# Kernel tuning notes

Measured on AMD Instinct MI355X. Metric: run time of the kernel, lower is better.

The kernel has to match this reference:

```python
import jax, jax.numpy as jnp
import numpy as np

NUM_QUBITS = 12
NUM_LAYERS = 4
N_CLASSES = 10
BATCH = 512
BN_EPS = 1e-5


def _apply_1q(state, U, wire):
    """Apply a 1-qubit gate U on `wire`. state: (B,)+(2,)*n; U: (2,2) or (B,2,2)."""
    state = jnp.moveaxis(state, wire + 1, -1)
    if U.ndim == 3:
        out = jnp.einsum('bij,b...j->b...i', U, state)
    else:
        out = jnp.einsum('ij,b...j->b...i', U, state)
    return jnp.moveaxis(out, -1, wire + 1)


def _apply_cnot(state, ctrl, tgt):
    s = jnp.moveaxis(state, (ctrl + 1, tgt + 1), (-2, -1))
    # where control bit == 1, flip the target axis
    s = jnp.concatenate([s[..., 0:1, :], s[..., 1:2, ::-1]], axis=-2)
    return jnp.moveaxis(s, (-2, -1), (ctrl + 1, tgt + 1))


def _rot(phi, theta, omega):
    """PennyLane Rot(phi, theta, omega) = RZ(omega) RY(theta) RZ(phi)."""
    c = jnp.cos(theta / 2)
    s = jnp.sin(theta / 2)
    row0 = jnp.stack([jnp.exp(-1j * (phi + omega) / 2) * c,
                      -jnp.exp(1j * (phi - omega) / 2) * s])
    row1 = jnp.stack([jnp.exp(-1j * (phi - omega) / 2) * s,
                      jnp.exp(1j * (phi + omega) / 2) * c])
    return jnp.stack([row0, row1]).astype(jnp.complex64)


def _circuit(x, weights):
    """Batched state-vector sim of the data-reuploading VQC.
    x: (B, n_qubits) angles; weights: (L, n_qubits, 3). Returns (B, N_CLASSES) <Z_i>."""
    B = x.shape[0]
    state = jnp.zeros((B,) + (2,) * NUM_QUBITS, jnp.complex64)
    state = state.at[(slice(None),) + (0,) * NUM_QUBITS].set(1.0)
    half = (x * 0.5).astype(jnp.float32)
    for l in range(NUM_LAYERS):
        w = weights[l]
        # angle embedding (RY(x_q) on each wire) -- batched gate, differs per sample
        for q in range(NUM_QUBITS):
            c = jnp.cos(half[:, q])
            s = jnp.sin(half[:, q])
            U = jnp.stack([jnp.stack([c, -s], -1),
                           jnp.stack([s, c], -1)], -2).astype(jnp.complex64)  # (B,2,2)
            state = _apply_1q(state, U, q)
        # one StronglyEntangling layer: Rot per wire (shared across batch)
        for q in range(NUM_QUBITS):
            state = _apply_1q(state, _rot(w[q, 0], w[q, 1], w[q, 2]), q)
        # ring of CNOTs (range 1)
        for q in range(NUM_QUBITS):
            state = _apply_cnot(state, q, (q + 1) % NUM_QUBITS)
    probs = jnp.abs(state) ** 2  # (B,)+(2,)*n, float32
    all_axes = tuple(range(1, NUM_QUBITS + 1))
    expz = []
    for i in range(N_CLASSES):
        axes = tuple(a for a in all_axes if a != i + 1)
        p = probs.sum(axis=axes)  # (B, 2) marginal of qubit i
        expz.append(p[:, 0] - p[:, 1])
    return jnp.stack(expz, axis=-1)  # (B, N_CLASSES)


def setup_inputs() -> dict:
    key = jax.random.key(0)
    k1, k2 = jax.random.split(key)
    x = jax.random.normal(k1, (BATCH, NUM_QUBITS), dtype=jnp.float32)
    weights = 0.01 * jax.random.uniform(k2, (NUM_LAYERS, NUM_QUBITS, 3), dtype=jnp.float32)
    bias = jnp.zeros((N_CLASSES,), jnp.float32)
    gamma = jnp.ones((N_CLASSES,), jnp.float32)
    beta = jnp.zeros((N_CLASSES,), jnp.float32)
    return {"x": x, "weights": weights, "bias": bias, "gamma": gamma, "beta": beta}


def reference(x, weights, bias, gamma, beta):
    expz = _circuit(x, weights)
    probs = jax.nn.softmax(expz + bias, axis=-1)
    # BatchNorm1d (training mode): biased batch statistics, affine
    mu = probs.mean(axis=0)
    var = probs.var(axis=0)
    return (probs - mu) / jnp.sqrt(var + BN_EPS) * gamma + beta
```

## Files before the change

### kernel.cpp

```cpp
#include <hip/hip_runtime.h>
#include <math.h>

#define NQ 12
#define NL 4
#define NC 10
#define NB 512
#define BN_EPS 1e-5f

typedef float v2f __attribute__((ext_vector_type(2)));

__device__ __forceinline__ void bfly(v2f& A, v2f& B,
    v2f c0, v2f c1, v2f c2, v2f c3, v2f c4, v2f c5, v2f c6, v2f c7)
{
    const v2f As = A.yx, Bs = B.yx;
    const v2f An = __builtin_elementwise_fma(c0, A,
                   __builtin_elementwise_fma(c1, As,
                   __builtin_elementwise_fma(c2, B, c3 * Bs)));
    const v2f Bn = __builtin_elementwise_fma(c4, A,
                   __builtin_elementwise_fma(c5, As,
                   __builtin_elementwise_fma(c6, B, c7 * Bs)));
    A = An; B = Bn;
}

__global__ __launch_bounds__(256) void vqc_kernel(
    const float* __restrict__ x, const float* __restrict__ w,
    const float* __restrict__ bias, float* __restrict__ probs)
{
    __shared__ v2f buf[2][4096];
    __shared__ __align__(16) float gm[48][16];
    __shared__ float red[4*NC];

    const int b = blockIdx.x;
    const int t = threadIdx.x;

    if (t < 48) {
        const int l = t / NQ, q = t % NQ;
        const float xq = 0.5f * x[b*NQ + q];
        const float cx = cosf(xq), sx = sinf(xq);
        const int wi = (l*NQ + q)*3;
        const float phi = w[wi], tht = w[wi+1], om = w[wi+2];
        const float ct = cosf(0.5f*tht), st = sinf(0.5f*tht);
        const float aa = 0.5f*(phi + om), dd = 0.5f*(phi - om);
        const float ca = cosf(aa), sa = sinf(aa);
        const float cd = cosf(dd), sd = sinf(dd);
        const float u00r =  ca*ct, u00i = -sa*ct;
        const float u01r = -cd*st, u01i = -sd*st;
        const float u10r =  cd*st, u10i = -sd*st;
        const float u11r =  ca*ct, u11i =  sa*ct;
        const float m00r = u00r*cx + u01r*sx, m00i = u00i*cx + u01i*sx;
        const float m01r = u01r*cx - u00r*sx, m01i = u01i*cx - u00i*sx;
        const float m10r = u10r*cx + u11r*sx, m10i = u10i*cx + u11i*sx;
        const float m11r = u11r*cx - u10r*sx, m11i = u11i*cx - u10i*sx;
        float* gp = gm[t];
        gp[0]  =  m00r; gp[1]  = m00r;
        gp[2]  = -m00i; gp[3]  = m00i;
        gp[4]  =  m01r; gp[5]  = m01r;
        gp[6]  = -m01i; gp[7]  = m01i;
        gp[8]  =  m10r; gp[9]  = m10r;
        gp[10] = -m10i; gp[11] = m10i;
        gp[12] =  m11r; gp[13] = m11r;
        gp[14] = -m11i; gp[15] = m11i;
    }
    __syncthreads();

    v2f a[16];
    #pragma unroll
    for (int r = 0; r < 16; ++r) a[r] = (v2f){0.f, 0.f};
    if (t == 0) a[0].x = 1.f;

    const int tl = t & 15, th4 = t >> 4;
    const int phit = t ^ th4;
    const int vAB = (th4 << 8) | (tl ^ (th4 * 17));
    const int wBC = (tl << 8) | ((th4 ^ tl) * 17);

    const unsigned b0_ = t & 1u, b1_ = (t>>1)&1u, b2_ = (t>>2)&1u, b3_ = (t>>3)&1u,
                   b4_ = (t>>4)&1u, b5_ = (t>>5)&1u, b6_ = (t>>6)&1u, b7_ = (t>>7)&1u;
    const unsigned P7 = b7_, P6 = P7^b6_, P5 = P6^b5_, P4 = P5^b4_,
                   P3 = P4^b3_, P2 = P3^b2_, P1 = P2^b1_, T = P1^b0_;
    const unsigned base_j = ((T ^ b7_) << 11) | (P6 << 10) | (P5 << 9) | (P4 << 8)
                          | (P3 << 7) | (P2 << 6) | (P1 << 5) | (T << 4)
                          | (T ? 0xFu : 0u);
    const unsigned rA = (base_j >> 8) & 15u;
    const unsigned tA = base_j & 255u;
    const unsigned baseCA = (rA << 8) | ((tA ^ (tA >> 4)) ^ (rA * 17u));

    #define STAGE(base) \
        _Pragma("unroll") \
        for (int g = 0; g < 4; ++g) { \
            const v2f* cp = (const v2f*)gm[(base) + 3 - g]; \
            const v2f c0=cp[0],c1=cp[1],c2=cp[2],c3=cp[3], \
                      c4=cp[4],c5=cp[5],c6=cp[6],c7=cp[7]; \
            const int bit = 1 << g; \
            _Pragma("unroll") \
            for (int r0 = 0; r0 < 16; ++r0) \
                if (!(r0 & bit)) bfly(a[r0], a[r0|bit], c0,c1,c2,c3,c4,c5,c6,c7); \
        }

    int pb = 0;
    #pragma unroll
    for (int l = 0; l < NL; ++l) {
        STAGE(l*12)
        {
            v2f* bp = buf[pb]; pb ^= 1;
            #pragma unroll
            for (int r = 0; r < 16; ++r) bp[vAB ^ (r*17)] = a[r];
            __syncthreads();
            #pragma unroll
            for (int r = 0; r < 16; ++r) a[r] = bp[(r<<8) | (phit ^ (r*17))];
        }

        STAGE(l*12 + 4)
        {
            v2f* bp = buf[pb]; pb ^= 1;
            #pragma unroll
            for (int r = 0; r < 16; ++r) bp[wBC ^ r] = a[r];
            __syncthreads();
            #pragma unroll
            for (int r = 0; r < 16; ++r) a[r] = bp[(r<<8) | (phit ^ (r*17))];
        }

        STAGE(l*12 + 8)
        if (l < NL-1) {
            v2f* bp = buf[pb]; pb ^= 1;
            #pragma unroll
            for (int r = 0; r < 16; ++r) {
                const unsigned k3 = (r>>3)&1u;
                const unsigned k2 = k3 ^ ((r>>2)&1u);
                const unsigned k1 = k2 ^ ((r>>1)&1u);
                const unsigned k0 = k1 ^ (r&1u);
                const unsigned K  = (k3<<3)|(k2<<2)|(k1<<1)|k0;
                const unsigned d  = K ^ (k0 * 0x888u);
                bp[baseCA ^ d] = a[r];
            }
            __syncthreads();
            #pragma unroll
            for (int r = 0; r < 16; ++r) a[r] = bp[(r<<8) | (phit ^ (r*17))];
        }
    }

    const float S0 = (T ^ b7_) ? -1.f : 1.f;
    const float S1 = P6 ? -1.f : 1.f;
    const float S2 = P5 ? -1.f : 1.f;
    const float S3 = P4 ? -1.f : 1.f;
    const float S4 = P3 ? -1.f : 1.f;
    const float S5 = P2 ? -1.f : 1.f;
    const float S6 = P1 ? -1.f : 1.f;
    const float S7 = T  ? -1.f : 1.f;
    const float S8 = T  ? -1.f : 1.f;
    const float S9 = T  ? -1.f : 1.f;

    float acc[NC];
    #pragma unroll
    for (int c = 0; c < NC; ++c) acc[c] = 0.f;
    #pragma unroll
    for (int r = 0; r < 16; ++r) {
        const float p = a[r].x*a[r].x + a[r].y*a[r].y;
        const int r3 = (r>>3)&1, r2 = (r>>2)&1, r1 = (r>>1)&1, r0b = r&1;
        const int par = r3 ^ r2 ^ r1 ^ r0b;
        acc[0] += (par        ? -S0 : S0) * p;
        acc[1] += S1 * p;
        acc[2] += S2 * p;
        acc[3] += S3 * p;
        acc[4] += S4 * p;
        acc[5] += S5 * p;
        acc[6] += S6 * p;
        acc[7] += S7 * p;
        acc[8] += (r3         ? -S8 : S8) * p;
        acc[9] += ((r3 ^ r2)  ? -S9 : S9) * p;
    }
    #pragma unroll
    for (int off = 32; off >= 1; off >>= 1) {
        #pragma unroll
        for (int c = 0; c < NC; ++c)
            acc[c] += __shfl_down(acc[c], off, 64);
    }
    const int wave = t >> 6, lane = t & 63;
    if (lane == 0) {
        #pragma unroll
        for (int c = 0; c < NC; ++c) red[wave*NC + c] = acc[c];
    }
    __syncthreads();
    if (t == 0) {
        float ez[NC];
        float mx = -1e30f;
        #pragma unroll
        for (int c = 0; c < NC; ++c) {
            ez[c] = red[c] + red[NC + c] + red[2*NC + c] + red[3*NC + c] + bias[c];
            mx = fmaxf(mx, ez[c]);
        }
        float sum = 0.f;
        #pragma unroll
        for (int c = 0; c < NC; ++c) { ez[c] = expf(ez[c] - mx); sum += ez[c]; }
        const float inv = 1.f / sum;
        #pragma unroll
        for (int c = 0; c < NC; ++c) probs[b*NC + c] = ez[c] * inv;
    }
}

__global__ __launch_bounds__(256) void bn_kernel(
    float* __restrict__ probs, const float* __restrict__ gamma,
    const float* __restrict__ beta)
{
    const int c = blockIdx.x;
    const int t = threadIdx.x;
    const float v0 = probs[t*NC + c];
    const float v1 = probs[(t + 256)*NC + c];
    float s  = v0 + v1;
    float ss = v0*v0 + v1*v1;
    #pragma unroll
    for (int off = 32; off >= 1; off >>= 1) {
        s  += __shfl_down(s,  off, 64);
        ss += __shfl_down(ss, off, 64);
    }
    __shared__ float sm[8];
    __shared__ float stat[2];
    const int wave = t >> 6, lane = t & 63;
    if (lane == 0) { sm[wave] = s; sm[4 + wave] = ss; }
    __syncthreads();
    if (t == 0) {
        const float S  = sm[0] + sm[1] + sm[2] + sm[3];
        const float SS = sm[4] + sm[5] + sm[6] + sm[7];
        const float mu  = S * (1.f/512.f);
        const float var = SS * (1.f/512.f) - mu*mu;
        stat[0] = mu;
        stat[1] = 1.f / sqrtf(var + BN_EPS);
    }
    __syncthreads();
    const float mu = stat[0], inv = stat[1];
    const float g = gamma[c], bt = beta[c];
    probs[t*NC + c]         = (v0 - mu) * inv * g + bt;
    probs[(t + 256)*NC + c] = (v1 - mu) * inv * g + bt;
}

extern "C" void kernel_launch(void* const* d_in, const int* in_sizes, int n_in,
                              void* d_out, int out_size, void* d_ws, size_t ws_size,
                              hipStream_t stream) {
    const float* x     = (const float*)d_in[0];
    const float* w     = (const float*)d_in[1];
    const float* bias  = (const float*)d_in[2];
    const float* gamma = (const float*)d_in[3];
    const float* beta  = (const float*)d_in[4];
    float* out = (float*)d_out;

    vqc_kernel<<<NB, 256, 0, stream>>>(x, w, bias, out);
    bn_kernel<<<NC, 256, 0, stream>>>(out, gamma, beta);
}
```

Baseline: 86.91 us.

## Split state vector over 512 threads with 8 amplitudes each and radix-8 stages

Moves from 256 threads holding 16 amplitudes (radix-16 stages, three LDS transposes per layer) to 512 threads holding 8 amplitudes (radix-8 stages, four transposes per layer) with a new XOR swizzle. The CNOT-ring permutation is now computed with a prefix-XOR formula, and the final Z-expectation reduction is rebuilt around per-thread parity sums. The goal is more parallelism and lower register pressure per block, at the cost of one extra shared-memory round trip and barrier per layer.

```diff
diff --git a/kernel.cpp b/kernel.cpp
--- a/kernel.cpp
+++ b/kernel.cpp
@@ -22,13 +22,13 @@
     A = An; B = Bn;
 }
 
-__global__ __launch_bounds__(256) void vqc_kernel(
+__global__ __launch_bounds__(512, 4) void vqc_kernel(
     const float* __restrict__ x, const float* __restrict__ w,
     const float* __restrict__ bias, float* __restrict__ probs)
 {
     __shared__ v2f buf[2][4096];
     __shared__ __align__(16) float gm[48][16];
-    __shared__ float red[4*NC];
+    __shared__ float red[8*NC];
 
     const int b = blockIdx.x;
     const int t = threadIdx.x;
@@ -63,111 +63,100 @@
     }
     __syncthreads();
 
-    v2f a[16];
-    #pragma unroll
-    for (int r = 0; r < 16; ++r) a[r] = (v2f){0.f, 0.f};
+    v2f a[8];
+    #pragma unroll
+    for (int r = 0; r < 8; ++r) a[r] = (v2f){0.f, 0.f};
     if (t == 0) a[0].x = 1.f;
 
-    const int tl = t & 15, th4 = t >> 4;
-    const int phit = t ^ th4;
-    const int vAB = (th4 << 8) | (tl ^ (th4 * 17));
-    const int wBC = (tl << 8) | ((th4 ^ tl) * 17);
-
-    const unsigned b0_ = t & 1u, b1_ = (t>>1)&1u, b2_ = (t>>2)&1u, b3_ = (t>>3)&1u,
-                   b4_ = (t>>4)&1u, b5_ = (t>>5)&1u, b6_ = (t>>6)&1u, b7_ = (t>>7)&1u;
-    const unsigned P7 = b7_, P6 = P7^b6_, P5 = P6^b5_, P4 = P5^b4_,
-                   P3 = P4^b3_, P2 = P3^b2_, P1 = P2^b1_, T = P1^b0_;
-    const unsigned base_j = ((T ^ b7_) << 11) | (P6 << 10) | (P5 << 9) | (P4 << 8)
-                          | (P3 << 7) | (P2 << 6) | (P1 << 5) | (T << 4)
-                          | (T ? 0xFu : 0u);
-    const unsigned rA = (base_j >> 8) & 15u;
-    const unsigned tA = base_j & 255u;
-    const unsigned baseCA = (rA << 8) | ((tA ^ (tA >> 4)) ^ (rA * 17u));
-
-    #define STAGE(base) \
+    const unsigned tu = (unsigned)t;
+    const unsigned tw = tu >> 6;
+    const unsigned baseB = (tw << 9) | (tu & 63u);
+    const unsigned baseC = (tw << 9) | (((tu >> 3) & 7u) << 6) | (tu & 7u);
+    const unsigned baseD = (tw << 9) | (((tu >> 3) & 7u) << 6) | ((tu & 7u) << 3);
+
+#define SWZ(i) ((i) ^ (((i) >> 4) & 15u))
+
+    #define STAGE(gbase) \
         _Pragma("unroll") \
-        for (int g = 0; g < 4; ++g) { \
-            const v2f* cp = (const v2f*)gm[(base) + 3 - g]; \
+        for (int g = 0; g < 3; ++g) { \
+            const v2f* cp = (const v2f*)gm[(gbase) + 2 - g]; \
             const v2f c0=cp[0],c1=cp[1],c2=cp[2],c3=cp[3], \
                       c4=cp[4],c5=cp[5],c6=cp[6],c7=cp[7]; \
             const int bit = 1 << g; \
             _Pragma("unroll") \
-            for (int r0 = 0; r0 < 16; ++r0) \
+            for (int r0 = 0; r0 < 8; ++r0) \
                 if (!(r0 & bit)) bfly(a[r0], a[r0|bit], c0,c1,c2,c3,c4,c5,c6,c7); \
         }
 
+    #define TRANS(IOLD, INEW) { \
+        v2f* bp = buf[pb]; pb ^= 1; \
+        _Pragma("unroll") \
+        for (int r = 0; r < 8; ++r) { const unsigned i_ = (IOLD); bp[SWZ(i_)] = a[r]; } \
+        __syncthreads(); \
+        _Pragma("unroll") \
+        for (int r = 0; r < 8; ++r) { const unsigned i_ = (INEW); a[r] = bp[SWZ(i_)]; } \
+    }
+
     int pb = 0;
     #pragma unroll
     for (int l = 0; l < NL; ++l) {
         STAGE(l*12)
-        {
-            v2f* bp = buf[pb]; pb ^= 1;
-            #pragma unroll
-            for (int r = 0; r < 16; ++r) bp[vAB ^ (r*17)] = a[r];
-            __syncthreads();
-            #pragma unroll
-            for (int r = 0; r < 16; ++r) a[r] = bp[(r<<8) | (phit ^ (r*17))];
-        }
-
-        STAGE(l*12 + 4)
-        {
-            v2f* bp = buf[pb]; pb ^= 1;
-            #pragma unroll
-            for (int r = 0; r < 16; ++r) bp[wBC ^ r] = a[r];
-            __syncthreads();
-            #pragma unroll
-            for (int r = 0; r < 16; ++r) a[r] = bp[(r<<8) | (phit ^ (r*17))];
-        }
-
-        STAGE(l*12 + 8)
+        TRANS(((unsigned)r << 9) | tu, baseB | ((unsigned)r << 6))
+        STAGE(l*12 + 3)
+        TRANS(baseB | ((unsigned)r << 6), baseC | ((unsigned)r << 3))
+        STAGE(l*12 + 6)
+        TRANS(baseC | ((unsigned)r << 3), baseD | (unsigned)r)
+        STAGE(l*12 + 9)
         if (l < NL-1) {
             v2f* bp = buf[pb]; pb ^= 1;
             #pragma unroll
-            for (int r = 0; r < 16; ++r) {
-                const unsigned k3 = (r>>3)&1u;
-                const unsigned k2 = k3 ^ ((r>>2)&1u);
-                const unsigned k1 = k2 ^ ((r>>1)&1u);
-                const unsigned k0 = k1 ^ (r&1u);
-                const unsigned K  = (k3<<3)|(k2<<2)|(k1<<1)|k0;
-                const unsigned d  = K ^ (k0 * 0x888u);
-                bp[baseCA ^ d] = a[r];
+            for (int r = 0; r < 8; ++r) {
+                unsigned i_ = baseD | (unsigned)r;
+                unsigned S = i_ ^ (i_ >> 1);
+                S ^= S >> 2; S ^= S >> 4; S ^= S >> 8;
+                const unsigned j = S ^ ((S & 1u) << 11);
+                bp[SWZ(j)] = a[r];
             }
             __syncthreads();
             #pragma unroll
-            for (int r = 0; r < 16; ++r) a[r] = bp[(r<<8) | (phit ^ (r*17))];
+            for (int r = 0; r < 8; ++r) {
+                const unsigned i_ = ((unsigned)r << 9) | tu;
+                a[r] = bp[SWZ(i_)];
+            }
         }
     }
 
-    const float S0 = (T ^ b7_) ? -1.f : 1.f;
-    const float S1 = P6 ? -1.f : 1.f;
-    const float S2 = P5 ? -1.f : 1.f;
-    const float S3 = P4 ? -1.f : 1.f;
-    const float S4 = P3 ? -1.f : 1.f;
-    const float S5 = P2 ? -1.f : 1.f;
-    const float S6 = P1 ? -1.f : 1.f;
-    const float S7 = T  ? -1.f : 1.f;
-    const float S8 = T  ? -1.f : 1.f;
-    const float S9 = T  ? -1.f : 1.f;
-
+    const unsigned t8 = (tu >> 8) & 1u;
+    const unsigned Q7 = t8 ^ ((tu >> 7) & 1u);
+    const unsigned Q6 = Q7 ^ ((tu >> 6) & 1u);
+    const unsigned Q5 = Q6 ^ ((tu >> 5) & 1u);
+    const unsigned Q4 = Q5 ^ ((tu >> 4) & 1u);
+    const unsigned Q3 = Q4 ^ ((tu >> 3) & 1u);
+    const unsigned Q2 = Q3 ^ ((tu >> 2) & 1u);
+    const unsigned Q1 = Q2 ^ ((tu >> 1) & 1u);
+    const unsigned Q0 = Q1 ^ (tu & 1u);
+
+    float psum = 0.f, pflip = 0.f, pflip2 = 0.f;
+    #pragma unroll
+    for (int r = 0; r < 8; ++r) {
+        const float p = a[r].x*a[r].x + a[r].y*a[r].y;
+        const int pr = ((r>>2) ^ (r>>1) ^ r) & 1;
+        psum  += p;
+        pflip  += pr      ? -p : p;
+        pflip2 += (r & 4) ? -p : p;
+    }
     float acc[NC];
-    #pragma unroll
-    for (int c = 0; c < NC; ++c) acc[c] = 0.f;
-    #pragma unroll
-    for (int r = 0; r < 16; ++r) {
-        const float p = a[r].x*a[r].x + a[r].y*a[r].y;
-        const int r3 = (r>>3)&1, r2 = (r>>2)&1, r1 = (r>>1)&1, r0b = r&1;
-        const int par = r3 ^ r2 ^ r1 ^ r0b;
-        acc[0] += (par        ? -S0 : S0) * p;
-        acc[1] += S1 * p;
-        acc[2] += S2 * p;
-        acc[3] += S3 * p;
-        acc[4] += S4 * p;
-        acc[5] += S5 * p;
-        acc[6] += S6 * p;
-        acc[7] += S7 * p;
-        acc[8] += (r3         ? -S8 : S8) * p;
-        acc[9] += ((r3 ^ r2)  ? -S9 : S9) * p;
-    }
+    acc[0] = ((t8 ^ Q0) ? -1.f : 1.f) * pflip;
+    acc[1] = (Q7 ? -1.f : 1.f) * psum;
+    acc[2] = (Q6 ? -1.f : 1.f) * psum;
+    acc[3] = (Q5 ? -1.f : 1.f) * psum;
+    acc[4] = (Q4 ? -1.f : 1.f) * psum;
+    acc[5] = (Q3 ? -1.f : 1.f) * psum;
+    acc[6] = (Q2 ? -1.f : 1.f) * psum;
+    acc[7] = (Q1 ? -1.f : 1.f) * psum;
+    acc[8] = (Q0 ? -1.f : 1.f) * psum;
+    acc[9] = (Q0 ? -1.f : 1.f) * pflip2;
+
     #pragma unroll
     for (int off = 32; off >= 1; off >>= 1) {
         #pragma unroll
@@ -185,8 +174,11 @@
         float mx = -1e30f;
         #pragma unroll
         for (int c = 0; c < NC; ++c) {
-            ez[c] = red[c] + red[NC + c] + red[2*NC + c] + red[3*NC + c] + bias[c];
-            mx = fmaxf(mx, ez[c]);
+            float s = bias[c];
+            #pragma unroll
+            for (int wv = 0; wv < 8; ++wv) s += red[wv*NC + c];
+            ez[c] = s;
+            mx = fmaxf(mx, s);
         }
         float sum = 0.f;
         #pragma unroll
@@ -242,6 +234,6 @@
     const float* beta  = (const float*)d_in[4];
     float* out = (float*)d_out;
 
-    vqc_kernel<<<NB, 256, 0, stream>>>(x, w, bias, out);
+    vqc_kernel<<<NB, 512, 0, stream>>>(x, w, bias, out);
     bn_kernel<<<NC, 256, 0, stream>>>(out, gamma, beta);
 }
```

Result: slower. 88.74 us (+2.1%).

## Fuse batchnorm into VQC kernel via last-block atomic counter

Applied to the files above, without the earlier changes.

Removes the separate batchnorm kernel launch. Each block increments a global counter after writing its softmax output, and the last block to finish computes per-class batch statistics and normalizes all rows in place. This adds a memset of the counter before the launch, plus a fence and atomic in every block. The serialized BN step now runs on a single block, where before it was spread over 10 blocks.

```diff
diff --git a/kernel.cpp b/kernel.cpp
--- a/kernel.cpp
+++ b/kernel.cpp
@@ -24,11 +24,15 @@
 
 __global__ __launch_bounds__(256) void vqc_kernel(
     const float* __restrict__ x, const float* __restrict__ w,
-    const float* __restrict__ bias, float* __restrict__ probs)
+    const float* __restrict__ bias, const float* __restrict__ gamma,
+    const float* __restrict__ beta, unsigned* __restrict__ ctr,
+    float* __restrict__ probs)
 {
     __shared__ v2f buf[2][4096];
     __shared__ __align__(16) float gm[48][16];
     __shared__ float red[4*NC];
+    __shared__ float bnS[4][NC], bnSS[4][NC], bnstat[2][NC];
+    __shared__ unsigned lastflag;
 
     const int b = blockIdx.x;
     const int t = threadIdx.x;
@@ -195,41 +199,53 @@
         #pragma unroll
         for (int c = 0; c < NC; ++c) probs[b*NC + c] = ez[c] * inv;
     }
-}
-
-__global__ __launch_bounds__(256) void bn_kernel(
-    float* __restrict__ probs, const float* __restrict__ gamma,
-    const float* __restrict__ beta)
-{
-    const int c = blockIdx.x;
-    const int t = threadIdx.x;
-    const float v0 = probs[t*NC + c];
-    const float v1 = probs[(t + 256)*NC + c];
-    float s  = v0 + v1;
-    float ss = v0*v0 + v1*v1;
+
+    __threadfence();
+    if (t == 0) lastflag = (atomicAdd(ctr, 1u) == (unsigned)(NB - 1));
+    __syncthreads();
+    if (!lastflag) return;
+    __threadfence();
+
+    float v0[NC], v1[NC], ps[NC], pss[NC];
+    const float* r0p = probs + t*NC;
+    const float* r1p = probs + (t + 256)*NC;
+    #pragma unroll
+    for (int c = 0; c < NC; ++c) {
+        v0[c] = r0p[c]; v1[c] = r1p[c];
+        ps[c]  = v0[c] + v1[c];
+        pss[c] = v0[c]*v0[c] + v1[c]*v1[c];
+    }
     #pragma unroll
     for (int off = 32; off >= 1; off >>= 1) {
-        s  += __shfl_down(s,  off, 64);
-        ss += __shfl_down(ss, off, 64);
-    }
-    __shared__ float sm[8];
-    __shared__ float stat[2];
-    const int wave = t >> 6, lane = t & 63;
-    if (lane == 0) { sm[wave] = s; sm[4 + wave] = ss; }
-    __syncthreads();
-    if (t == 0) {
-        const float S  = sm[0] + sm[1] + sm[2] + sm[3];
-        const float SS = sm[4] + sm[5] + sm[6] + sm[7];
+        #pragma unroll
+        for (int c = 0; c < NC; ++c) {
+            ps[c]  += __shfl_down(ps[c],  off, 64);
+            pss[c] += __shfl_down(pss[c], off, 64);
+        }
+    }
+    if (lane == 0) {
+        #pragma unroll
+        for (int c = 0; c < NC; ++c) { bnS[wave][c] = ps[c]; bnSS[wave][c] = pss[c]; }
+    }
+    __syncthreads();
+    if (t < NC) {
+        const float S  = bnS[0][t] + bnS[1][t] + bnS[2][t] + bnS[3][t];
+        const float SS = bnSS[0][t] + bnSS[1][t] + bnSS[2][t] + bnSS[3][t];
         const float mu  = S * (1.f/512.f);
         const float var = SS * (1.f/512.f) - mu*mu;
-        stat[0] = mu;
-        stat[1] = 1.f / sqrtf(var + BN_EPS);
-    }
-    __syncthreads();
-    const float mu = stat[0], inv = stat[1];
-    const float g = gamma[c], bt = beta[c];
-    probs[t*NC + c]         = (v0 - mu) * inv * g + bt;
-    probs[(t + 256)*NC + c] = (v1 - mu) * inv * g + bt;
+        bnstat[0][t] = mu;
+        bnstat[1][t] = 1.f / sqrtf(var + BN_EPS);
+    }
+    __syncthreads();
+    float* w0p = probs + t*NC;
+    float* w1p = probs + (t + 256)*NC;
+    #pragma unroll
+    for (int c = 0; c < NC; ++c) {
+        const float mu = bnstat[0][c], inv = bnstat[1][c];
+        const float g = gamma[c], bt = beta[c];
+        w0p[c] = (v0[c] - mu) * inv * g + bt;
+        w1p[c] = (v1[c] - mu) * inv * g + bt;
+    }
 }
 
 extern "C" void kernel_launch(void* const* d_in, const int* in_sizes, int n_in,
@@ -242,6 +258,7 @@
     const float* beta  = (const float*)d_in[4];
     float* out = (float*)d_out;
 
-    vqc_kernel<<<NB, 256, 0, stream>>>(x, w, bias, out);
-    bn_kernel<<<NC, 256, 0, stream>>>(out, gamma, beta);
+    hipMemsetAsync(d_ws, 0, sizeof(unsigned), stream);
+    vqc_kernel<<<NB, 256, 0, stream>>>(x, w, bias, gamma, beta,
+                                       (unsigned*)d_ws, out);
 }
```

Result: slower. 120.1 us (+38.2%).
